# Optimization experiments

Hardware: AMD Instinct MI355X
Metric: run time of the kernel (lower is better)

Reference implementation:

```python
import math
import jax, jax.numpy as jnp
import numpy as np

H_CYCLES, L_CYCLES = 3, 2
STD = 0.02


def setup_inputs() -> dict:
    key = jax.random.key(0)
    ks = jax.random.split(key, 11)
    D, nh, mult, V, T, B = 512, 8, 64, 8192, 512, 4
    N = mult * D // nh
    def nrm(k, shape):
        return jax.random.normal(k, shape, jnp.float32) * STD
    return {
        "idx": jax.random.randint(ks[0], (B, T), 0, V),
        "embed_w": nrm(ks[1], (V, D)),
        "h_enc": nrm(ks[2], (nh, D, N)),
        "h_enc_v": nrm(ks[3], (nh, D, N)),
        "h_dec": nrm(ks[4], (nh * N, D)),
        "l_enc": nrm(ks[5], (nh, D, N)),
        "l_enc_v": nrm(ks[6], (nh, D, N)),
        "l_dec": nrm(ks[7], (nh * N, D)),
        "lm_head": nrm(ks[8], (D, V)),
        "h_init": nrm(ks[9], (D,)),
        "l_init": nrm(ks[10], (D,)),
    }


def _ln(x, eps=1e-5):
    # LayerNorm without affine params (elementwise_affine=False)
    m = jnp.mean(x, axis=-1, keepdims=True)
    v = jnp.var(x, axis=-1, keepdims=True)
    return (x - m) * jax.lax.rsqrt(v + eps)


def _rope_tables(T, N):
    # freqs with even-quantized exponent, angles wrapped mod 1 then scaled by 2*pi
    q = jnp.floor(jnp.arange(N, dtype=jnp.float32) / 2.0) * 2.0
    freqs = 1.0 / jnp.power(2.0 ** 16, q / N) / (2.0 * math.pi)
    phases = jnp.arange(T, dtype=jnp.float32)[:, None] * freqs[None, :]
    ang = (phases % 1.0) * (2.0 * math.pi)
    return jnp.cos(ang), jnp.sin(ang)  # each (T, N)


def _rope(v, cos, sin):
    # v: (B, nh, T, N); interleaved rotation as in torch stack/view trick
    v_rot = jnp.stack((-v[..., 1::2], v[..., ::2]), axis=-1).reshape(v.shape)
    return v * cos + v_rot * sin


def _attn(x_sparse, Vmat, cos, sin):
    # x_sparse: (B, nh, T, N); Vmat: (B, T, D)
    N = x_sparse.shape[-1]
    T = x_sparse.shape[-2]
    QR = _rope(x_sparse, cos, sin)
    scores = jnp.einsum('bhtn,bhsn->bhts', QR, QR) * (N ** -0.5)
    mask = jnp.tril(jnp.ones((T, T), dtype=bool), k=-1)  # strict lower triangle
    scores = jnp.where(mask, scores, 0.0)
    return jnp.einsum('bhts,bsd->bhtd', scores, Vmat)  # (B, nh, T, D)


def _block(x, inj, enc, enc_v, dec, cos, sin):
    # x, inj: (B, 1, T, D)
    B, _, T, D = x.shape
    nh, _, N = enc.shape
    xi = _ln(x + inj)[:, 0]  # (B, T, D)
    x_sparse = jax.nn.relu(jnp.einsum('btd,hdn->bhtn', xi, enc))
    yKV = _ln(_attn(x_sparse, xi, cos, sin))  # (B, nh, T, D)
    y_sparse = jax.nn.relu(jnp.einsum('bhtd,hdn->bhtn', yKV, enc_v))
    xy = (x_sparse * y_sparse).transpose(0, 2, 1, 3).reshape(B, 1, T, nh * N)
    y = _ln(xy @ dec)  # (B, 1, T, D)
    return _ln(x + y)


def reference(idx, embed_w, h_enc, h_enc_v, h_dec, l_enc, l_enc_v, l_dec,
              lm_head, h_init, l_init):
    B, T = idx.shape
    D = embed_w.shape[1]
    N = l_enc.shape[-1]
    cos, sin = _rope_tables(T, N)
    inp = _ln(embed_w[idx])[:, None]  # (B, 1, T, D)
    z_H = jnp.broadcast_to(h_init, (B, 1, T, D))
    z_L = jnp.broadcast_to(l_init, (B, 1, T, D))
    for h in range(H_CYCLES):
        for l in range(L_CYCLES):
            if not (h == H_CYCLES - 1 and l == L_CYCLES - 1):
                z_L = _block(z_L, z_H + inp, l_enc, l_enc_v, l_dec, cos, sin)
        if h < H_CYCLES - 1:
            z_H = _block(z_H, z_L, h_enc, h_enc_v, h_dec, cos, sin)
    z_L = _block(z_L, z_H + inp, l_enc, l_enc_v, l_dec, cos, sin)
    z_H = _block(z_H, z_L, h_enc, h_enc_v, h_dec, cos, sin)
    logits = z_H[:, 0] @ lm_head  # (B, T, vocab)
    return logits
```

## Files before the change

kernel.cpp:

```cpp
#include <hip/hip_runtime.h>

typedef _Float16 f16;
typedef __attribute__((ext_vector_type(8))) _Float16 f16x8;
typedef __attribute__((ext_vector_type(4))) float f32x4;
typedef __attribute__((ext_vector_type(4))) int i32x4;

#define D_  512
#define NH_ 8
#define NS_ 4096
#define TT_ 512
#define BB_ 4
#define VV_ 8192
#define HN_ 32768
#define BT_ 2048


__device__ __forceinline__ void gl16(const void* g, void* l) {
  __builtin_amdgcn_global_load_lds((const __attribute__((address_space(1))) void*)g,
                                   (__attribute__((address_space(3))) void*)l, 16, 0, 0);
}

__device__ __forceinline__ void gemm_core(const f16* __restrict__ A, const f16* __restrict__ B,
    int lda, int ldb, int nk, char* As, char* Bs, f32x4 acc[4][4]) {
  int tid = threadIdx.x;
  int l = tid & 63, wid = tid >> 6;
  int wm = wid >> 1, wn = wid & 1;
  int row0 = tid >> 3, g0 = tid & 7;
  for (int kt = 0; kt < nk; ++kt) {
    __syncthreads();
#pragma unroll
    for (int it = 0; it < 4; ++it) {
      int row = row0 + 32 * it;
      int gs = g0 ^ (row & 7);
      int wb = (wid * 64 + it * 256) * 16;
      gl16(A + (size_t)row * lda + gs * 8, As + wb);
      gl16(B + (size_t)row * ldb + gs * 8, Bs + wb);
    }
    __syncthreads();
    A += 64; B += 64;
#pragma unroll
    for (int kh = 0; kh < 2; ++kh) {
      f16x8 af[4], bfr[4];
#pragma unroll
      for (int m = 0; m < 4; ++m) {
        int row = wm * 64 + m * 16 + (l & 15);
        int off = row * 128 + ((kh * 64 + (l >> 4) * 16) ^ ((row & 7) << 4));
        af[m] = *(const f16x8*)(As + off);
      }
#pragma unroll
      for (int n = 0; n < 4; ++n) {
        int row = wn * 64 + n * 16 + (l & 15);
        int off = row * 128 + ((kh * 64 + (l >> 4) * 16) ^ ((row & 7) << 4));
        bfr[n] = *(const f16x8*)(Bs + off);
      }
#pragma unroll
      for (int m = 0; m < 4; ++m)
#pragma unroll
        for (int n = 0; n < 4; ++n)
          acc[m][n] = __builtin_amdgcn_mfma_f32_16x16x32_f16(af[m], bfr[n], acc[m][n], 0, 0, 0);
    }
  }
}


__global__ __launch_bounds__(256, 4) void k_gemm_xs(
    const f16* __restrict__ xi, const f16* __restrict__ encT,
    const f16* __restrict__ csT, f16* __restrict__ qr) {
  __shared__ i32x4 As4[1024], Bs4[1024];
  int bid = blockIdx.x;
  int swz = (bid & 7) * 512 + (bid >> 3);
  int mt = swz & 15, nt = (swz >> 4) & 31, h = swz >> 9;
  const f16* A = xi + (size_t)mt * 128 * D_;
  const f16* B = encT + ((size_t)h * NS_ + nt * 128) * D_;
  f32x4 acc[4][4] = {};
  gemm_core(A, B, D_, D_, D_ / 64, (char*)As4, (char*)Bs4, acc);
  int l = threadIdx.x & 63, wid = threadIdx.x >> 6;
  int wm = wid >> 1, wn = wid & 1;
  int r04 = (l >> 4) * 4, c0 = l & 15;
  int b = (mt * 128) >> 9;
  int tbase = (mt * 128) & (TT_ - 1);
#pragma unroll
  for (int m = 0; m < 4; ++m)
#pragma unroll
    for (int n = 0; n < 4; ++n)
#pragma unroll
      for (int r = 0; r < 4; ++r) {
        int row = wm * 64 + m * 16 + r04 + r;
        int col = wn * 64 + n * 16 + c0;
        int t = tbase + row;
        int nn = nt * 128 + col;
        float xsv = fmaxf(acc[m][n][r], 0.f);
        float prt = __shfl_xor(xsv, 1);
        int ci = 2 * (t * NS_ + nn);
        float c = (float)csT[ci], s = (float)csT[ci + 1];
        float qv = xsv * c + ((nn & 1) ? prt : -prt) * s;
        size_t o = (((size_t)b * NH_ + h) * TT_ + t) * NS_ + nn;
        qr[o] = (f16)qv;
      }
}

__global__ __launch_bounds__(256, 4) void k_gemm_scores(
    const f16* __restrict__ qr, f16* __restrict__ scores) {
  __shared__ i32x4 As4[1024], Bs4[1024];
  int bid = blockIdx.x;
  int swz = (bid & 7) * 40 + (bid >> 3);
  int x = swz % 10, z = swz / 10;
  int mt = (x >= 6) ? 3 : (x >= 3) ? 2 : (x >= 1) ? 1 : 0;
  int nt = x - mt * (mt + 1) / 2;
  const f16* base = qr + (size_t)z * TT_ * NS_;
  const f16* A = base + (size_t)mt * 128 * NS_;
  const f16* B = base + (size_t)nt * 128 * NS_;
  f32x4 acc[4][4] = {};
  gemm_core(A, B, NS_, NS_, NS_ / 64, (char*)As4, (char*)Bs4, acc);
  int l = threadIdx.x & 63, wid = threadIdx.x >> 6;
  int wm = wid >> 1, wn = wid & 1;
  int r04 = (l >> 4) * 4, c0 = l & 15;
  f16* outp = scores + (size_t)z * TT_ * TT_;
#pragma unroll
  for (int m = 0; m < 4; ++m)
#pragma unroll
    for (int n = 0; n < 4; ++n)
#pragma unroll
      for (int r = 0; r < 4; ++r) {
        int t = mt * 128 + wm * 64 + m * 16 + r04 + r;
        int s_ = nt * 128 + wn * 64 + n * 16 + c0;
        float v = (t > s_) ? acc[m][n][r] * 0.015625f : 0.f;
        outp[(size_t)t * TT_ + s_] = (f16)v;
      }
}

__global__ __launch_bounds__(256, 4) void k_gemm_attn(
    const f16* __restrict__ scores, const f16* __restrict__ xiT, f16* __restrict__ attn) {
  __shared__ i32x4 As4[1024], Bs4[1024];
  int bid = blockIdx.x;
  int swz = (bid & 7) * 64 + (bid >> 3);
  int mt = swz & 3, ntd = (swz >> 2) & 3, z = swz >> 4;
  int b = z >> 3;
  const f16* A = scores + (size_t)z * TT_ * TT_ + (size_t)mt * 128 * TT_;
  const f16* B = xiT + (size_t)b * D_ * TT_ + (size_t)ntd * 128 * TT_;
  f32x4 acc[4][4] = {};
  gemm_core(A, B, TT_, TT_, 2 * mt + 2, (char*)As4, (char*)Bs4, acc);
  int l = threadIdx.x & 63, wid = threadIdx.x >> 6;
  int wm = wid >> 1, wn = wid & 1;
  int r04 = (l >> 4) * 4, c0 = l & 15;
#pragma unroll
  for (int m = 0; m < 4; ++m)
#pragma unroll
    for (int n = 0; n < 4; ++n)
#pragma unroll
      for (int r = 0; r < 4; ++r) {
        int t = mt * 128 + wm * 64 + m * 16 + r04 + r;
        int d = ntd * 128 + wn * 64 + n * 16 + c0;
        attn[((size_t)z * TT_ + t) * D_ + d] = (f16)acc[m][n][r];
      }
}

__global__ __launch_bounds__(256, 4) void k_gemm_xy(
    const f16* __restrict__ ykv, const f16* __restrict__ encvT,
    const f16* __restrict__ csT, f16* __restrict__ qrxy) {
  __shared__ i32x4 As4[1024], Bs4[1024];
  int bid = blockIdx.x;
  int swz = (bid & 7) * 512 + (bid >> 3);
  int mt = swz & 3, nt = (swz >> 2) & 31, z = swz >> 7;
  int h = z & 7;
  const f16* A = ykv + (size_t)z * TT_ * D_ + (size_t)mt * 128 * D_;
  const f16* B = encvT + ((size_t)h * NS_ + nt * 128) * D_;
  f32x4 acc[4][4] = {};
  gemm_core(A, B, D_, D_, D_ / 64, (char*)As4, (char*)Bs4, acc);
  int l = threadIdx.x & 63, wid = threadIdx.x >> 6;
  int wm = wid >> 1, wn = wid & 1;
  int r04 = (l >> 4) * 4, c0 = l & 15;
#pragma unroll
  for (int m = 0; m < 4; ++m)
#pragma unroll
    for (int n = 0; n < 4; ++n)
#pragma unroll
      for (int r = 0; r < 4; ++r) {
        int t = mt * 128 + wm * 64 + m * 16 + r04 + r;
        int nn = nt * 128 + wn * 64 + n * 16 + c0;
        float ys = fmaxf(acc[m][n][r], 0.f);
        size_t o = ((size_t)z * TT_ + t) * NS_ + nn;
        float qv = (float)qrxy[o];
        float prt = __shfl_xor(qv, 1);
        int ci = 2 * (t * NS_ + nn);
        float c = (float)csT[ci], s = (float)csT[ci + 1];
        float xsv = (nn & 1) ? (qv * c - prt * s) : (qv * c + prt * s);
        qrxy[o] = (f16)(xsv * ys);
      }
}

__global__ __launch_bounds__(256, 4) void k_gemm_ydec(
    const f16* __restrict__ xy, const f16* __restrict__ decT, f16* __restrict__ ypart) {
  __shared__ i32x4 As4[1024], Bs4[1024];
  int bid = blockIdx.x;
  int swz = (bid & 7) * 64 + (bid >> 3);
  int mt = swz & 15, nt = (swz >> 4) & 3, kz = swz >> 6;
  int b = mt >> 2, t0 = (mt & 3) * 128;
  const f16* A = xy + ((size_t)(b * NH_ + kz) * TT_ + t0) * NS_;
  const f16* B = decT + (size_t)nt * 128 * HN_ + (size_t)kz * NS_;
  f32x4 acc[4][4] = {};
  gemm_core(A, B, NS_, HN_, NS_ / 64, (char*)As4, (char*)Bs4, acc);
  int l = threadIdx.x & 63, wid = threadIdx.x >> 6;
  int wm = wid >> 1, wn = wid & 1;
  int r04 = (l >> 4) * 4, c0 = l & 15;
  f16* outp = ypart + (size_t)kz * BT_ * D_;
#pragma unroll
  for (int m = 0; m < 4; ++m)
#pragma unroll
    for (int n = 0; n < 4; ++n)
#pragma unroll
      for (int r = 0; r < 4; ++r) {
        int R = mt * 128 + wm * 64 + m * 16 + r04 + r;
        int c = nt * 128 + wn * 64 + n * 16 + c0;
        outp[(size_t)R * D_ + c] = (f16)acc[m][n][r];
      }
}

__global__ __launch_bounds__(256, 4) void k_gemm_logits(
    const f16* __restrict__ zbf, const f16* __restrict__ lmT, float* __restrict__ outp) {
  __shared__ i32x4 As4[1024], Bs4[1024];
  int bid = blockIdx.x;
  int swz = (bid & 7) * 128 + (bid >> 3);
  int mt = swz & 15, nt = swz >> 4;
  const f16* A = zbf + (size_t)mt * 128 * D_;
  const f16* B = lmT + (size_t)nt * 128 * D_;
  f32x4 acc[4][4] = {};
  gemm_core(A, B, D_, D_, D_ / 64, (char*)As4, (char*)Bs4, acc);
  int l = threadIdx.x & 63, wid = threadIdx.x >> 6;
  int wm = wid >> 1, wn = wid & 1;
  int r04 = (l >> 4) * 4, c0 = l & 15;
#pragma unroll
  for (int m = 0; m < 4; ++m)
#pragma unroll
    for (int n = 0; n < 4; ++n)
#pragma unroll
      for (int r = 0; r < 4; ++r) {
        int R = mt * 128 + wm * 64 + m * 16 + r04 + r;
        int v = nt * 128 + wn * 64 + n * 16 + c0;
        outp[(size_t)R * VV_ + v] = acc[m][n][r];
      }
}


__device__ __forceinline__ float block_sum(float v, float* sb) {
#pragma unroll
  for (int o = 32; o > 0; o >>= 1) v += __shfl_xor(v, o);
  int w = threadIdx.x >> 6;
  if ((threadIdx.x & 63) == 0) sb[w] = v;
  __syncthreads();
  float r = sb[0] + sb[1] + sb[2] + sb[3];
  __syncthreads();
  return r;
}

struct F2 { float x, y; };
__device__ __forceinline__ F2 ln2(float x, float y, float* sb) {
  float mean = block_sum(x + y, sb) * (1.f / 512.f);
  float dx = x - mean, dy = y - mean;
  float var = block_sum(dx * dx + dy * dy, sb) * (1.f / 512.f);
  float rs = rsqrtf(var + 1e-5f);
  F2 o; o.x = dx * rs; o.y = dy * rs; return o;
}

__global__ __launch_bounds__(256) void k_tables(f16* __restrict__ csT) {
  int i = blockIdx.x * 256 + threadIdx.x;
  int t = i >> 12, n = i & (NS_ - 1);
  float q = (float)(n & ~1);
  float freq = exp2f(-16.f * q / 4096.f) * 0.15915494309189535f;
  float ph = (float)t * freq;
  ph -= floorf(ph);
  float ang = ph * 6.283185307179586f;
  csT[2 * i]     = (f16)cosf(ang);
  csT[2 * i + 1] = (f16)sinf(ang);
}

__global__ void k_transpose(const float* __restrict__ in, f16* __restrict__ outp, int R, int C) {
  __shared__ float tile[32][33];
  size_t mo = (size_t)blockIdx.z * R * C;
  in += mo; outp += mo;
  int c0 = blockIdx.x * 32, r0 = blockIdx.y * 32;
#pragma unroll
  for (int i = threadIdx.y; i < 32; i += 8)
    tile[i][threadIdx.x] = in[(size_t)(r0 + i) * C + c0 + threadIdx.x];
  __syncthreads();
#pragma unroll
  for (int i = threadIdx.y; i < 32; i += 8)
    outp[(size_t)(c0 + i) * R + r0 + threadIdx.x] = (f16)tile[threadIdx.x][i];
}

__global__ __launch_bounds__(256) void k_embed_ln(const int* __restrict__ idx,
    const float* __restrict__ emb, f16* __restrict__ inp) {
  __shared__ float sb[4];
  int r = blockIdx.x;
  const float* e = emb + (size_t)idx[r] * D_;
  int d = threadIdx.x * 2;
  F2 v = ln2(e[d], e[d + 1], sb);
  inp[(size_t)r * D_ + d]     = (f16)v.x;
  inp[(size_t)r * D_ + d + 1] = (f16)v.y;
}

__global__ __launch_bounds__(256) void k_init(const float* __restrict__ hi,
    const float* __restrict__ li, f16* __restrict__ zH, f16* __restrict__ zL) {
  size_t i = (size_t)blockIdx.x * 256 + threadIdx.x;
  zH[i] = (f16)hi[i & (D_ - 1)];
  zL[i] = (f16)li[i & (D_ - 1)];
}

__global__ __launch_bounds__(256) void k_ln_xi(const f16* __restrict__ x,
    const f16* __restrict__ a1, const f16* __restrict__ a2,
    f16* __restrict__ xi, f16* __restrict__ xiT) {
  __shared__ float sb[4];
  int r = blockIdx.x;
  int d = threadIdx.x * 2;
  size_t o = (size_t)r * D_ + d;
  float vx = (float)x[o] + (float)a1[o];
  float vy = (float)x[o + 1] + (float)a1[o + 1];
  if (a2) { vx += (float)a2[o]; vy += (float)a2[o + 1]; }
  F2 v = ln2(vx, vy, sb);
  xi[o] = (f16)v.x; xi[o + 1] = (f16)v.y;
  int b = r >> 9, t = r & (TT_ - 1);
  xiT[((size_t)b * D_ + d) * TT_ + t]     = (f16)v.x;
  xiT[((size_t)b * D_ + d + 1) * TT_ + t] = (f16)v.y;
}

__global__ __launch_bounds__(256) void k_ln_rows(const f16* __restrict__ in, f16* __restrict__ outp) {
  __shared__ float sb[4];
  int r = blockIdx.x;
  int d = threadIdx.x * 2;
  size_t o = (size_t)r * D_ + d;
  F2 v = ln2((float)in[o], (float)in[o + 1], sb);
  outp[o] = (f16)v.x; outp[o + 1] = (f16)v.y;
}

__global__ __launch_bounds__(256) void k_ln_y_out(const f16* __restrict__ ypart,
    f16* __restrict__ z) {
  __shared__ float sb[4];
  int r = blockIdx.x;
  int d = threadIdx.x * 2;
  size_t o = (size_t)r * D_ + d;
  float sx = 0.f, sy = 0.f;
#pragma unroll
  for (int k = 0; k < 8; ++k) {
    sx += (float)ypart[(size_t)k * BT_ * D_ + o];
    sy += (float)ypart[(size_t)k * BT_ * D_ + o + 1];
  }
  F2 yl = ln2(sx, sy, sb);
  float vx = (float)z[o] + yl.x, vy = (float)z[o + 1] + yl.y;
  F2 zo = ln2(vx, vy, sb);
  z[o] = (f16)zo.x; z[o + 1] = (f16)zo.y;
}


extern "C" void kernel_launch(void* const* d_in, const int* in_sizes, int n_in,
                              void* d_out, int out_size, void* d_ws, size_t ws_size,
                              hipStream_t stream) {
  (void)in_sizes; (void)n_in; (void)out_size; (void)ws_size;
  const int*   idx    = (const int*)  d_in[0];
  const float* emb    = (const float*)d_in[1];
  const float* h_enc  = (const float*)d_in[2];
  const float* h_encv = (const float*)d_in[3];
  const float* h_dec  = (const float*)d_in[4];
  const float* l_enc  = (const float*)d_in[5];
  const float* l_encv = (const float*)d_in[6];
  const float* l_dec  = (const float*)d_in[7];
  const float* lm     = (const float*)d_in[8];
  const float* h_init = (const float*)d_in[9];
  const float* l_init = (const float*)d_in[10];
  float* out = (float*)d_out;

  char* w = (char*)d_ws;
  size_t off = 0;
  auto alloc = [&](size_t n) { void* p = w + off; off += (n + 255) & ~(size_t)255; return p; };
  f16* csT    = (f16*)alloc(8388608);
  f16* encT   = (f16*)alloc(33554432);
  f16* encvT  = (f16*)alloc(33554432);
  f16* decT   = (f16*)alloc(33554432);
  f16* inp    = (f16*)alloc(2097152);
  f16* zH     = (f16*)alloc(2097152);
  f16* zL     = (f16*)alloc(2097152);
  f16* xi_bf  = (f16*)alloc(2097152);
  f16* xiT_bf = (f16*)alloc(2097152);
  f16* qrxy   = (f16*)alloc(134217728);

  f16* scoresB = (f16*)d_out;
  f16* attnP   = (f16*)((char*)d_out + 16777216);
  f16* ypart   = attnP;
  f16* ykv     = (f16*)((char*)d_out + 33554432);

  dim3 tb(32, 8);
  k_tables<<<8192, 256, 0, stream>>>(csT);
  k_embed_ln<<<2048, 256, 0, stream>>>(idx, emb, inp);
  k_init<<<4096, 256, 0, stream>>>(h_init, l_init, zH, zL);

  int cur = -1;
  auto setw = [&](int sel) {
    if (cur == sel) return;
    cur = sel;
    const float* e  = sel ? h_enc  : l_enc;
    const float* ev = sel ? h_encv : l_encv;
    const float* dc = sel ? h_dec  : l_dec;
    k_transpose<<<dim3(128, 16, 8), tb, 0, stream>>>(e,  encT,  512, 4096);
    k_transpose<<<dim3(128, 16, 8), tb, 0, stream>>>(ev, encvT, 512, 4096);
    k_transpose<<<dim3(16, 1024, 1), tb, 0, stream>>>(dc, decT, 32768, 512);
  };

  auto run_block = [&](f16* zx, const f16* a1, const f16* a2) {
    k_ln_xi<<<2048, 256, 0, stream>>>(zx, a1, a2, xi_bf, xiT_bf);
    k_gemm_xs<<<4096, 256, 0, stream>>>(xi_bf, encT, csT, qrxy);
    k_gemm_scores<<<320, 256, 0, stream>>>(qrxy, scoresB);
    k_gemm_attn<<<512, 256, 0, stream>>>(scoresB, xiT_bf, attnP);
    k_ln_rows<<<16384, 256, 0, stream>>>(attnP, ykv);
    k_gemm_xy<<<4096, 256, 0, stream>>>(ykv, encvT, csT, qrxy);
    k_gemm_ydec<<<512, 256, 0, stream>>>(qrxy, decT, ypart);
    k_ln_y_out<<<2048, 256, 0, stream>>>(ypart, zx);
  };

  for (int i = 0; i < 3; ++i) {
    setw(0);
    run_block(zL, inp, zH);
    run_block(zL, inp, zH);
    setw(1);
    run_block(zH, zL, (const f16*)nullptr);
  }
  k_transpose<<<dim3(256, 16, 1), tb, 0, stream>>>(lm, encT, 512, 8192);
  k_gemm_logits<<<1024, 256, 0, stream>>>(zH, encT, out);
}
```

Measured before the change: 4.551 ms.

## Keep both weight sets transposed resident and use wave-per-row LayerNorm kernels

When the workspace is large enough, the L and H weight sets and the LM head are each transposed into fp16 once, at the start, into separate buffers. This removes the repeated re-transposition of roughly 100 MB of weights on every H/L switch (six switches). The LayerNorm kernels are also rewritten so one wave handles one row with 16-byte vector loads and shuffle-only reductions, which drops the block-level syncs and shared memory. The costs are a larger workspace requirement and strided scalar stores for the transposed xi output.

```diff
diff --git a/kernel.cpp b/kernel.cpp
--- a/kernel.cpp
+++ b/kernel.cpp
@@ -44,14 +44,12 @@
 #pragma unroll
       for (int m = 0; m < 4; ++m) {
         int row = wm * 64 + m * 16 + (l & 15);
-        int off = row * 128 + ((kh * 64 + (l >> 4) * 16) ^ ((row & 7) << 4));
-        af[m] = *(const f16x8*)(As + off);
+        af[m] = *(const f16x8*)(As + row * 128 + ((kh * 64 + (l >> 4) * 16) ^ ((row & 7) << 4)));
       }
 #pragma unroll
       for (int n = 0; n < 4; ++n) {
         int row = wn * 64 + n * 16 + (l & 15);
-        int off = row * 128 + ((kh * 64 + (l >> 4) * 16) ^ ((row & 7) << 4));
-        bfr[n] = *(const f16x8*)(Bs + off);
+        bfr[n] = *(const f16x8*)(Bs + row * 128 + ((kh * 64 + (l >> 4) * 16) ^ ((row & 7) << 4)));
       }
 #pragma unroll
       for (int m = 0; m < 4; ++m)
@@ -242,24 +240,10 @@
 }
 
 
-__device__ __forceinline__ float block_sum(float v, float* sb) {
+__device__ __forceinline__ float wave_sum(float v) {
 #pragma unroll
   for (int o = 32; o > 0; o >>= 1) v += __shfl_xor(v, o);
-  int w = threadIdx.x >> 6;
-  if ((threadIdx.x & 63) == 0) sb[w] = v;
-  __syncthreads();
-  float r = sb[0] + sb[1] + sb[2] + sb[3];
-  __syncthreads();
-  return r;
-}
-
-struct F2 { float x, y; };
-__device__ __forceinline__ F2 ln2(float x, float y, float* sb) {
-  float mean = block_sum(x + y, sb) * (1.f / 512.f);
-  float dx = x - mean, dy = y - mean;
-  float var = block_sum(dx * dx + dy * dy, sb) * (1.f / 512.f);
-  float rs = rsqrtf(var + 1e-5f);
-  F2 o; o.x = dx * rs; o.y = dy * rs; return o;
+  return v;
 }
 
 __global__ __launch_bounds__(256) void k_tables(f16* __restrict__ csT) {
@@ -290,13 +274,26 @@
 
 __global__ __launch_bounds__(256) void k_embed_ln(const int* __restrict__ idx,
     const float* __restrict__ emb, f16* __restrict__ inp) {
-  __shared__ float sb[4];
-  int r = blockIdx.x;
-  const float* e = emb + (size_t)idx[r] * D_;
-  int d = threadIdx.x * 2;
-  F2 v = ln2(e[d], e[d + 1], sb);
-  inp[(size_t)r * D_ + d]     = (f16)v.x;
-  inp[(size_t)r * D_ + d + 1] = (f16)v.y;
+  int r = blockIdx.x * 4 + (threadIdx.x >> 6);
+  int lane = threadIdx.x & 63;
+  const float* e = emb + (size_t)idx[r] * D_ + lane * 8;
+  f32x4 e0 = *(const f32x4*)e;
+  f32x4 e1 = *(const f32x4*)(e + 4);
+  float v[8];
+#pragma unroll
+  for (int i = 0; i < 4; ++i) { v[i] = e0[i]; v[i + 4] = e1[i]; }
+  float s = 0.f;
+#pragma unroll
+  for (int i = 0; i < 8; ++i) s += v[i];
+  float mean = wave_sum(s) * (1.f / 512.f);
+  float q = 0.f;
+#pragma unroll
+  for (int i = 0; i < 8; ++i) { v[i] -= mean; q += v[i] * v[i]; }
+  float rs = rsqrtf(wave_sum(q) * (1.f / 512.f) + 1e-5f);
+  f16x8 ov;
+#pragma unroll
+  for (int i = 0; i < 8; ++i) ov[i] = (f16)(v[i] * rs);
+  *(f16x8*)(inp + (size_t)r * D_ + lane * 8) = ov;
 }
 
 __global__ __launch_bounds__(256) void k_init(const float* __restrict__ hi,
@@ -309,52 +306,102 @@
 __global__ __launch_bounds__(256) void k_ln_xi(const f16* __restrict__ x,
     const f16* __restrict__ a1, const f16* __restrict__ a2,
     f16* __restrict__ xi, f16* __restrict__ xiT) {
-  __shared__ float sb[4];
-  int r = blockIdx.x;
-  int d = threadIdx.x * 2;
-  size_t o = (size_t)r * D_ + d;
-  float vx = (float)x[o] + (float)a1[o];
-  float vy = (float)x[o + 1] + (float)a1[o + 1];
-  if (a2) { vx += (float)a2[o]; vy += (float)a2[o + 1]; }
-  F2 v = ln2(vx, vy, sb);
-  xi[o] = (f16)v.x; xi[o + 1] = (f16)v.y;
+  int r = blockIdx.x * 4 + (threadIdx.x >> 6);
+  int lane = threadIdx.x & 63;
+  size_t o = (size_t)r * D_ + lane * 8;
+  f16x8 xv = *(const f16x8*)(x + o);
+  f16x8 av = *(const f16x8*)(a1 + o);
+  float v[8];
+#pragma unroll
+  for (int i = 0; i < 8; ++i) v[i] = (float)xv[i] + (float)av[i];
+  if (a2) {
+    f16x8 bv = *(const f16x8*)(a2 + o);
+#pragma unroll
+    for (int i = 0; i < 8; ++i) v[i] += (float)bv[i];
+  }
+  float s = 0.f;
+#pragma unroll
+  for (int i = 0; i < 8; ++i) s += v[i];
+  float mean = wave_sum(s) * (1.f / 512.f);
+  float q = 0.f;
+#pragma unroll
+  for (int i = 0; i < 8; ++i) { v[i] -= mean; q += v[i] * v[i]; }
+  float rs = rsqrtf(wave_sum(q) * (1.f / 512.f) + 1e-5f);
+  f16x8 ov;
+#pragma unroll
+  for (int i = 0; i < 8; ++i) ov[i] = (f16)(v[i] * rs);
+  *(f16x8*)(xi + o) = ov;
   int b = r >> 9, t = r & (TT_ - 1);
-  xiT[((size_t)b * D_ + d) * TT_ + t]     = (f16)v.x;
-  xiT[((size_t)b * D_ + d + 1) * TT_ + t] = (f16)v.y;
+  int d0 = lane * 8;
+#pragma unroll
+  for (int i = 0; i < 8; ++i)
+    xiT[((size_t)b * D_ + d0 + i) * TT_ + t] = ov[i];
 }
 
 __global__ __launch_bounds__(256) void k_ln_rows(const f16* __restrict__ in, f16* __restrict__ outp) {
-  __shared__ float sb[4];
-  int r = blockIdx.x;
-  int d = threadIdx.x * 2;
-  size_t o = (size_t)r * D_ + d;
-  F2 v = ln2((float)in[o], (float)in[o + 1], sb);
-  outp[o] = (f16)v.x; outp[o + 1] = (f16)v.y;
+  int r = blockIdx.x * 4 + (threadIdx.x >> 6);
+  int lane = threadIdx.x & 63;
+  size_t o = (size_t)r * D_ + lane * 8;
+  f16x8 xv = *(const f16x8*)(in + o);
+  float v[8];
+#pragma unroll
+  for (int i = 0; i < 8; ++i) v[i] = (float)xv[i];
+  float s = 0.f;
+#pragma unroll
+  for (int i = 0; i < 8; ++i) s += v[i];
+  float mean = wave_sum(s) * (1.f / 512.f);
+  float q = 0.f;
+#pragma unroll
+  for (int i = 0; i < 8; ++i) { v[i] -= mean; q += v[i] * v[i]; }
+  float rs = rsqrtf(wave_sum(q) * (1.f / 512.f) + 1e-5f);
+  f16x8 ov;
+#pragma unroll
+  for (int i = 0; i < 8; ++i) ov[i] = (f16)(v[i] * rs);
+  *(f16x8*)(outp + o) = ov;
 }
 
 __global__ __launch_bounds__(256) void k_ln_y_out(const f16* __restrict__ ypart,
     f16* __restrict__ z) {
-  __shared__ float sb[4];
-  int r = blockIdx.x;
-  int d = threadIdx.x * 2;
-  size_t o = (size_t)r * D_ + d;
-  float sx = 0.f, sy = 0.f;
+  int r = blockIdx.x * 4 + (threadIdx.x >> 6);
+  int lane = threadIdx.x & 63;
+  size_t o = (size_t)r * D_ + lane * 8;
+  float v[8] = {};
 #pragma unroll
   for (int k = 0; k < 8; ++k) {
-    sx += (float)ypart[(size_t)k * BT_ * D_ + o];
-    sy += (float)ypart[(size_t)k * BT_ * D_ + o + 1];
-  }
-  F2 yl = ln2(sx, sy, sb);
-  float vx = (float)z[o] + yl.x, vy = (float)z[o + 1] + yl.y;
-  F2 zo = ln2(vx, vy, sb);
-  z[o] = (f16)zo.x; z[o + 1] = (f16)zo.y;
+    f16x8 p = *(const f16x8*)(ypart + (size_t)k * BT_ * D_ + o);
+#pragma unroll
+    for (int i = 0; i < 8; ++i) v[i] += (float)p[i];
+  }
+  float s = 0.f;
+#pragma unroll
+  for (int i = 0; i < 8; ++i) s += v[i];
+  float mean = wave_sum(s) * (1.f / 512.f);
+  float q = 0.f;
+#pragma unroll
+  for (int i = 0; i < 8; ++i) { v[i] -= mean; q += v[i] * v[i]; }
+  float rs = rsqrtf(wave_sum(q) * (1.f / 512.f) + 1e-5f);
+  f16x8 zv = *(const f16x8*)(z + o);
+#pragma unroll
+  for (int i = 0; i < 8; ++i) v[i] = (float)zv[i] + v[i] * rs;
+  s = 0.f;
+#pragma unroll
+  for (int i = 0; i < 8; ++i) s += v[i];
+  mean = wave_sum(s) * (1.f / 512.f);
+  q = 0.f;
+#pragma unroll
+  for (int i = 0; i < 8; ++i) { v[i] -= mean; q += v[i] * v[i]; }
+  rs = rsqrtf(wave_sum(q) * (1.f / 512.f) + 1e-5f);
+  f16x8 ov;
+#pragma unroll
+  for (int i = 0; i < 8; ++i) ov[i] = (f16)(v[i] * rs);
+  *(f16x8*)(z + o) = ov;
 }
 
 
 extern "C" void kernel_launch(void* const* d_in, const int* in_sizes, int n_in,
                               void* d_out, int out_size, void* d_ws, size_t ws_size,
                               hipStream_t stream) {
-  (void)in_sizes; (void)n_in; (void)out_size; (void)ws_size;
+  (void)in_sizes; (void)n_in; (void)out_size;
   const int*   idx    = (const int*)  d_in[0];
   const float* emb    = (const float*)d_in[1];
   const float* h_enc  = (const float*)d_in[2];
@@ -368,13 +415,26 @@
   const float* l_init = (const float*)d_in[10];
   float* out = (float*)d_out;
 
+  bool resident = ws_size >= ((size_t)352 << 20);
+
   char* w = (char*)d_ws;
   size_t off = 0;
   auto alloc = [&](size_t n) { void* p = w + off; off += (n + 255) & ~(size_t)255; return p; };
-  f16* csT    = (f16*)alloc(8388608);
-  f16* encT   = (f16*)alloc(33554432);
-  f16* encvT  = (f16*)alloc(33554432);
-  f16* decT   = (f16*)alloc(33554432);
+  f16* csT = (f16*)alloc(8388608);
+  f16 *encT[2], *encvT[2], *decT[2], *lmT;
+  if (resident) {
+    for (int s = 0; s < 2; ++s) {
+      encT[s]  = (f16*)alloc(33554432);
+      encvT[s] = (f16*)alloc(33554432);
+      decT[s]  = (f16*)alloc(33554432);
+    }
+    lmT = (f16*)alloc(8388608);
+  } else {
+    encT[0]  = encT[1]  = (f16*)alloc(33554432);
+    encvT[0] = encvT[1] = (f16*)alloc(33554432);
+    decT[0]  = decT[1]  = (f16*)alloc(33554432);
+    lmT = encT[0];
+  }
   f16* inp    = (f16*)alloc(2097152);
   f16* zH     = (f16*)alloc(2097152);
   f16* zL     = (f16*)alloc(2097152);
@@ -388,40 +448,50 @@
   f16* ykv     = (f16*)((char*)d_out + 33554432);
 
   dim3 tb(32, 8);
-  k_tables<<<8192, 256, 0, stream>>>(csT);
-  k_embed_ln<<<2048, 256, 0, stream>>>(idx, emb, inp);
-  k_init<<<4096, 256, 0, stream>>>(h_init, l_init, zH, zL);
-
-  int cur = -1;
-  auto setw = [&](int sel) {
-    if (cur == sel) return;
-    cur = sel;
+  auto transpose_set = [&](int sel) {
     const float* e  = sel ? h_enc  : l_enc;
     const float* ev = sel ? h_encv : l_encv;
     const float* dc = sel ? h_dec  : l_dec;
-    k_transpose<<<dim3(128, 16, 8), tb, 0, stream>>>(e,  encT,  512, 4096);
-    k_transpose<<<dim3(128, 16, 8), tb, 0, stream>>>(ev, encvT, 512, 4096);
-    k_transpose<<<dim3(16, 1024, 1), tb, 0, stream>>>(dc, decT, 32768, 512);
+    k_transpose<<<dim3(128, 16, 8), tb, 0, stream>>>(e,  encT[sel],  512, 4096);
+    k_transpose<<<dim3(128, 16, 8), tb, 0, stream>>>(ev, encvT[sel], 512, 4096);
+    k_transpose<<<dim3(16, 1024, 1), tb, 0, stream>>>(dc, decT[sel], 32768, 512);
   };
 
-  auto run_block = [&](f16* zx, const f16* a1, const f16* a2) {
-    k_ln_xi<<<2048, 256, 0, stream>>>(zx, a1, a2, xi_bf, xiT_bf);
-    k_gemm_xs<<<4096, 256, 0, stream>>>(xi_bf, encT, csT, qrxy);
+  k_tables<<<8192, 256, 0, stream>>>(csT);
+  k_embed_ln<<<512, 256, 0, stream>>>(idx, emb, inp);
+  k_init<<<4096, 256, 0, stream>>>(h_init, l_init, zH, zL);
+  if (resident) {
+    transpose_set(0);
+    transpose_set(1);
+    k_transpose<<<dim3(256, 16, 1), tb, 0, stream>>>(lm, lmT, 512, 8192);
+  }
+
+  int cur = -1;
+  auto setw = [&](int sel) {
+    if (resident || cur == sel) { cur = sel; return; }
+    cur = sel;
+    transpose_set(sel);
+  };
+
+  auto run_block = [&](f16* zx, const f16* a1, const f16* a2, int s) {
+    k_ln_xi<<<512, 256, 0, stream>>>(zx, a1, a2, xi_bf, xiT_bf);
+    k_gemm_xs<<<4096, 256, 0, stream>>>(xi_bf, encT[s], csT, qrxy);
     k_gemm_scores<<<320, 256, 0, stream>>>(qrxy, scoresB);
     k_gemm_attn<<<512, 256, 0, stream>>>(scoresB, xiT_bf, attnP);
-    k_ln_rows<<<16384, 256, 0, stream>>>(attnP, ykv);
-    k_gemm_xy<<<4096, 256, 0, stream>>>(ykv, encvT, csT, qrxy);
-    k_gemm_ydec<<<512, 256, 0, stream>>>(qrxy, decT, ypart);
-    k_ln_y_out<<<2048, 256, 0, stream>>>(ypart, zx);
+    k_ln_rows<<<4096, 256, 0, stream>>>(attnP, ykv);
+    k_gemm_xy<<<4096, 256, 0, stream>>>(ykv, encvT[s], csT, qrxy);
+    k_gemm_ydec<<<512, 256, 0, stream>>>(qrxy, decT[s], ypart);
+    k_ln_y_out<<<512, 256, 0, stream>>>(ypart, zx);
   };
 
   for (int i = 0; i < 3; ++i) {
     setw(0);
-    run_block(zL, inp, zH);
-    run_block(zL, inp, zH);
+    run_block(zL, inp, zH, 0);
+    run_block(zL, inp, zH, 0);
     setw(1);
-    run_block(zH, zL, (const f16*)nullptr);
-  }
-  k_transpose<<<dim3(256, 16, 1), tb, 0, stream>>>(lm, encT, 512, 8192);
-  k_gemm_logits<<<1024, 256, 0, stream>>>(zH, encT, out);
-}
+    run_block(zH, zL, (const f16*)nullptr, 1);
+  }
+  if (!resident)
+    k_transpose<<<dim3(256, 16, 1), tb, 0, stream>>>(lm, lmT, 512, 8192);
+  k_gemm_logits<<<1024, 256, 0, stream>>>(zH, lmT, out);
+}
```

Result: faster. 4.054 ms (-10.9%).
